# Performance work log

Hardware: AMD Instinct MI355X
Metric: run time of the kernel (lower is better)

The kernel has to match this reference:

```python
import jax, jax.numpy as jnp
import numpy as np

DIM = 768
NUM_HEADS = 12
LATENT_LEN = 32


def setup_inputs() -> dict:
    key = jax.random.key(0)
    k1, k2, k3, k4 = jax.random.split(key, 4)
    x = jax.random.normal(k1, (32, 4096, DIM), dtype=jnp.float32)
    latent = jax.random.normal(k2, (1, LATENT_LEN, DIM), dtype=jnp.float32) * 0.02
    # torch nn.Linear(dim, dim): weight [out, in], bias [out]
    bound = 1.0 / np.sqrt(DIM)
    v_w = jax.random.uniform(k3, (DIM, DIM), dtype=jnp.float32, minval=-bound, maxval=bound)
    v_b = jax.random.uniform(k4, (DIM,), dtype=jnp.float32, minval=-bound, maxval=bound)
    return {"x": x, "latent": latent, "v_w": v_w, "v_b": v_b}


def reference(x, latent, v_w, v_b):
    B, N, C = x.shape
    H = NUM_HEADS
    hd = C // H
    L = LATENT_LEN
    chunk = C // L
    scale = hd ** (-0.5)

    # q: [L, H, hd] from latent (shared across batch)
    q = latent[0].reshape(L, H, hd)
    # k: [B, N, H, hd]
    k = x.reshape(B, N, H, hd)
    # attn logits: [B, H, L, N]
    attn = jnp.einsum("lhd,bnhd->bhln", q * scale, k)
    attn = jax.nn.softmax(attn, axis=-1)
    attn = attn.mean(axis=1)  # [B, L, N] (head-mean before value matmul)

    # v: Linear then split channels by latent_len -> [B, L, N, chunk]
    v = (jnp.einsum("bnc,dc->bnd", x, v_w) + v_b).reshape(B, N, L, chunk)
    out = jnp.einsum("bln,blnc->blc", attn, v.transpose(0, 2, 1, 3))
    return out.reshape(B, 1, C)
```

## Files before the change

### kernel.cpp

```cpp
#include <hip/hip_runtime.h>
#include <cstdint>


typedef short bf16x8 __attribute__((ext_vector_type(8)));
typedef float f32x4 __attribute__((ext_vector_type(4)));

#define MFMA16(a, b, c) __builtin_amdgcn_mfma_f32_16x16x32_bf16((a), (b), (c), 0, 0, 0)

__device__ __forceinline__ unsigned short f2bf(float f) {
    union { float f; uint32_t u; } v; v.f = f;
    uint32_t u = v.u;
    u += 0x7FFFu + ((u >> 16) & 1u);
    return (unsigned short)(u >> 16);
}

template <int MODE>
__global__ __launch_bounds__(256)
void attn_sw_kernel(const float* __restrict__ x, const float* __restrict__ latent,
                    float* __restrict__ g_sums, const float* __restrict__ g_rs,
                    unsigned short* __restrict__ g_W)
{
    const int b   = blockIdx.x >> 6;
    const int n0  = (blockIdx.x & 63) << 6;
    const int tid = threadIdx.x;
    const int wv  = tid >> 6;
    const int lane = tid & 63;
    const int quad = lane >> 4;
    const int lc   = lane & 15;

    __shared__ unsigned short q_lds[32][72];
    __shared__ unsigned short x_lds[64][72];
    __shared__ float red_lds[384];

    if (MODE == 0) {
        for (int i = tid; i < 384; i += 256) red_lds[i] = 0.0f;
    } else {
        for (int i = tid; i < 384; i += 256) red_lds[i] = g_rs[b * 384 + i];
    }

    float acc0[4] = {0.f, 0.f, 0.f, 0.f};
    float acc1[4] = {0.f, 0.f, 0.f, 0.f};

    for (int h = 0; h < 12; ++h) {
        __syncthreads();
        for (int i = tid; i < 512; i += 256) {
            int l = i >> 4, f4 = i & 15;
            float4 qv = *(const float4*)&latent[l * 768 + h * 64 + f4 * 4];
            ushort4 qb;
            qb.x = f2bf(qv.x * 0.125f); qb.y = f2bf(qv.y * 0.125f);
            qb.z = f2bf(qv.z * 0.125f); qb.w = f2bf(qv.w * 0.125f);
            *(ushort4*)&q_lds[l][f4 * 4] = qb;
        }
        for (int i = tid; i < 1024; i += 256) {
            int n = i >> 4, f4 = i & 15;
            float4 xv = *(const float4*)&x[(b * 4096 + n0 + n) * 768 + h * 64 + f4 * 4];
            ushort4 xb;
            xb.x = f2bf(xv.x); xb.y = f2bf(xv.y);
            xb.z = f2bf(xv.z); xb.w = f2bf(xv.w);
            *(ushort4*)&x_lds[n][f4 * 4] = xb;
        }
        __syncthreads();

        bf16x8 a00 = *(const bf16x8*)&q_lds[lc][quad * 8];
        bf16x8 a01 = *(const bf16x8*)&q_lds[lc][32 + quad * 8];
        bf16x8 a10 = *(const bf16x8*)&q_lds[16 + lc][quad * 8];
        bf16x8 a11 = *(const bf16x8*)&q_lds[16 + lc][32 + quad * 8];
        bf16x8 b0  = *(const bf16x8*)&x_lds[wv * 16 + lc][quad * 8];
        bf16x8 b1  = *(const bf16x8*)&x_lds[wv * 16 + lc][32 + quad * 8];

        f32x4 c0 = {0.f, 0.f, 0.f, 0.f};
        f32x4 c1 = {0.f, 0.f, 0.f, 0.f};
        c0 = MFMA16(a00, b0, c0);
        c0 = MFMA16(a01, b1, c0);
        c1 = MFMA16(a10, b0, c1);
        c1 = MFMA16(a11, b1, c1);

        #pragma unroll
        for (int r = 0; r < 4; ++r) {
            float e0 = __expf(c0[r]);
            float e1 = __expf(c1[r]);
            if (MODE == 0) {
                float v0 = e0, v1 = e1;
                #pragma unroll
                for (int m = 1; m < 16; m <<= 1) {
                    v0 += __shfl_xor(v0, m);
                    v1 += __shfl_xor(v1, m);
                }
                if (lc == 0) {
                    atomicAdd(&red_lds[h * 32 + quad * 4 + r], v0);
                    atomicAdd(&red_lds[h * 32 + 16 + quad * 4 + r], v1);
                }
            } else {
                acc0[r] += e0 * red_lds[h * 32 + quad * 4 + r];
                acc1[r] += e1 * red_lds[h * 32 + 16 + quad * 4 + r];
            }
        }
    }

    if (MODE == 0) {
        __syncthreads();
        for (int i = tid; i < 384; i += 256)
            atomicAdd(&g_sums[b * 384 + i], red_lds[i]);
    } else {
        const int n = n0 + wv * 16 + lc;
        #pragma unroll
        for (int r = 0; r < 4; ++r) {
            g_W[(b * 32 + quad * 4 + r) * 4096 + n]      = f2bf(acc0[r]);
            g_W[(b * 32 + 16 + quad * 4 + r) * 4096 + n] = f2bf(acc1[r]);
        }
    }
}

__global__ __launch_bounds__(256)
void invert_kernel(const float* __restrict__ sums, float* __restrict__ rs)
{
    int i = blockIdx.x * 256 + threadIdx.x;
    if (i < 12288) rs[i] = 1.0f / (12.0f * sums[i]);
}

__global__ __launch_bounds__(64)
void yacc_kernel(const float* __restrict__ x, const unsigned short* __restrict__ W,
                 float* __restrict__ yws)
{
    const int bx  = blockIdx.x;
    const int b   = bx / 48;
    const int rem = bx - b * 48;
    const int ct  = rem % 12;
    const int g   = rem / 12;
    const int lane = threadIdx.x;
    const int quad = lane >> 4;
    const int lc   = lane & 15;
    const int c0   = ct * 64;
    const int nb   = g * 1024;

    const float* xb = x + b * 4096 * 768;
    const unsigned short* Wb = W + b * 32 * 4096;

    f32x4 acc[2][4];
    #pragma unroll
    for (int t = 0; t < 2; ++t)
        #pragma unroll
        for (int s = 0; s < 4; ++s) acc[t][s] = (f32x4){0.f, 0.f, 0.f, 0.f};

    for (int kk = 0; kk < 1024; kk += 32) {
        const int n = nb + kk + quad * 8;
        bf16x8 a0 = *(const bf16x8*)&Wb[lc * 4096 + n];
        bf16x8 a1 = *(const bf16x8*)&Wb[(16 + lc) * 4096 + n];
        #pragma unroll
        for (int s = 0; s < 4; ++s) {
            const float* xp = xb + n * 768 + c0 + s * 16 + lc;
            bf16x8 bb;
            #pragma unroll
            for (int j = 0; j < 8; ++j) bb[j] = (short)f2bf(xp[j * 768]);
            acc[0][s] = MFMA16(a0, bb, acc[0][s]);
            acc[1][s] = MFMA16(a1, bb, acc[1][s]);
        }
    }

    float* yp = yws + ((g * 32 + b) * 32) * 768;
    #pragma unroll
    for (int t = 0; t < 2; ++t)
        #pragma unroll
        for (int s = 0; s < 4; ++s)
            #pragma unroll
            for (int r = 0; r < 4; ++r) {
                int l = t * 16 + quad * 4 + r;
                int c = c0 + s * 16 + lc;
                yp[l * 768 + c] = acc[t][s][r];
            }
}

__global__ __launch_bounds__(256)
void out_kernel(const float* __restrict__ yws, const float* __restrict__ vw,
                const float* __restrict__ vb, float* __restrict__ out)
{
    const int b = blockIdx.x >> 5;
    const int l = blockIdx.x & 31;
    const int tid = threadIdx.x;
    __shared__ float y_lds[768];
    for (int c = tid; c < 768; c += 256) {
        float v = 0.f;
        #pragma unroll
        for (int g = 0; g < 4; ++g)
            v += yws[((g * 32 + b) * 32 + l) * 768 + c];
        y_lds[c] = v;
    }
    __syncthreads();
    const int wv = tid >> 6, lane = tid & 63;
    for (int i = wv; i < 24; i += 4) {
        const int row = l * 24 + i;
        const float* wr = vw + row * 768;
        float p = 0.f;
        #pragma unroll
        for (int j = 0; j < 12; ++j)
            p += y_lds[j * 64 + lane] * wr[j * 64 + lane];
        #pragma unroll
        for (int m = 1; m < 64; m <<= 1) p += __shfl_xor(p, m);
        if (lane == 0) out[b * 768 + row] = p + vb[row];
    }
}

extern "C" void kernel_launch(void* const* d_in, const int* in_sizes, int n_in,
                              void* d_out, int out_size, void* d_ws, size_t ws_size,
                              hipStream_t stream)
{
    const float* x      = (const float*)d_in[0];
    const float* latent = (const float*)d_in[1];
    const float* vw     = (const float*)d_in[2];
    const float* vb     = (const float*)d_in[3];
    float* out = (float*)d_out;

    char* ws = (char*)d_ws;
    float*          sums = (float*)ws;
    float*          rs   = (float*)(ws + 49152);
    unsigned short* W    = (unsigned short*)(ws + 98304);
    float*          yws  = (float*)(ws + 98304 + 8388608);

    hipMemsetAsync(sums, 0, 12288 * sizeof(float), stream);
    attn_sw_kernel<0><<<dim3(2048), dim3(256), 0, stream>>>(x, latent, sums, nullptr, nullptr);
    invert_kernel<<<dim3(48), dim3(256), 0, stream>>>(sums, rs);
    attn_sw_kernel<1><<<dim3(2048), dim3(256), 0, stream>>>(x, latent, nullptr, rs, W);
    yacc_kernel<<<dim3(1536), dim3(64), 0, stream>>>(x, W, yws);
    out_kernel<<<dim3(1024), dim3(256), 0, stream>>>(yws, vw, vb, out);
}
```

Before: 713.1 us.

## Materialize exp logits once instead of recomputing attention in two passes

Replaces the two-pass attention kernel (sum pass plus weighted pass, each rereading all of x) with a single pass that writes bf16 exp-logits to a 96MB workspace. A second kernel then reduces the per-head sums and forms the head-mean weights. This removes one full read of x (about 400MB) and its bf16 conversion, at the cost of writing and reading back roughly 100MB of intermediates. Two smaller changes come with it: bf16 conversion now truncates with a perm instruction instead of round-to-nearest, which may affect accuracy, and the yacc kernel is split into twice as many blocks over N for more parallelism.

```diff
diff --git a/kernel.cpp b/kernel.cpp
--- a/kernel.cpp
+++ b/kernel.cpp
@@ -7,18 +7,18 @@
 
 #define MFMA16(a, b, c) __builtin_amdgcn_mfma_f32_16x16x32_bf16((a), (b), (c), 0, 0, 0)
 
-__device__ __forceinline__ unsigned short f2bf(float f) {
-    union { float f; uint32_t u; } v; v.f = f;
-    uint32_t u = v.u;
-    u += 0x7FFFu + ((u >> 16) & 1u);
-    return (unsigned short)(u >> 16);
-}
-
-template <int MODE>
+__device__ __forceinline__ uint32_t pk_bf16(float a, float b) {
+    return __builtin_amdgcn_perm(__float_as_uint(b), __float_as_uint(a), 0x07060302u);
+}
+__device__ __forceinline__ unsigned short bf16_trunc(float f) {
+    return (unsigned short)(__float_as_uint(f) >> 16);
+}
+__device__ __forceinline__ float bf16_lo(uint32_t u) { return __uint_as_float(u << 16); }
+__device__ __forceinline__ float bf16_hi(uint32_t u) { return __uint_as_float(u & 0xffff0000u); }
+
 __global__ __launch_bounds__(256)
-void attn_sw_kernel(const float* __restrict__ x, const float* __restrict__ latent,
-                    float* __restrict__ g_sums, const float* __restrict__ g_rs,
-                    unsigned short* __restrict__ g_W)
+void k1_logits(const float* __restrict__ x, const float* __restrict__ latent,
+               unsigned short* __restrict__ E)
 {
     const int b   = blockIdx.x >> 6;
     const int n0  = (blockIdx.x & 63) << 6;
@@ -30,34 +30,26 @@
 
     __shared__ unsigned short q_lds[32][72];
     __shared__ unsigned short x_lds[64][72];
-    __shared__ float red_lds[384];
-
-    if (MODE == 0) {
-        for (int i = tid; i < 384; i += 256) red_lds[i] = 0.0f;
-    } else {
-        for (int i = tid; i < 384; i += 256) red_lds[i] = g_rs[b * 384 + i];
-    }
-
-    float acc0[4] = {0.f, 0.f, 0.f, 0.f};
-    float acc1[4] = {0.f, 0.f, 0.f, 0.f};
+
+    const int n = n0 + wv * 16 + lc;
 
     for (int h = 0; h < 12; ++h) {
         __syncthreads();
         for (int i = tid; i < 512; i += 256) {
             int l = i >> 4, f4 = i & 15;
             float4 qv = *(const float4*)&latent[l * 768 + h * 64 + f4 * 4];
-            ushort4 qb;
-            qb.x = f2bf(qv.x * 0.125f); qb.y = f2bf(qv.y * 0.125f);
-            qb.z = f2bf(qv.z * 0.125f); qb.w = f2bf(qv.w * 0.125f);
-            *(ushort4*)&q_lds[l][f4 * 4] = qb;
+            uint2 p;
+            p.x = pk_bf16(qv.x * 0.125f, qv.y * 0.125f);
+            p.y = pk_bf16(qv.z * 0.125f, qv.w * 0.125f);
+            *(uint2*)&q_lds[l][f4 * 4] = p;
         }
         for (int i = tid; i < 1024; i += 256) {
-            int n = i >> 4, f4 = i & 15;
-            float4 xv = *(const float4*)&x[(b * 4096 + n0 + n) * 768 + h * 64 + f4 * 4];
-            ushort4 xb;
-            xb.x = f2bf(xv.x); xb.y = f2bf(xv.y);
-            xb.z = f2bf(xv.z); xb.w = f2bf(xv.w);
-            *(ushort4*)&x_lds[n][f4 * 4] = xb;
+            int nn = i >> 4, f4 = i & 15;
+            float4 xv = *(const float4*)&x[(b * 4096 + n0 + nn) * 768 + h * 64 + f4 * 4];
+            uint2 p;
+            p.x = pk_bf16(xv.x, xv.y);
+            p.y = pk_bf16(xv.z, xv.w);
+            *(uint2*)&x_lds[nn][f4 * 4] = p;
         }
         __syncthreads();
 
@@ -75,47 +67,73 @@
         c1 = MFMA16(a10, b0, c1);
         c1 = MFMA16(a11, b1, c1);
 
+        unsigned short* Eh = E + (size_t)((b * 12 + h) * 32) * 4096;
         #pragma unroll
         for (int r = 0; r < 4; ++r) {
-            float e0 = __expf(c0[r]);
-            float e1 = __expf(c1[r]);
-            if (MODE == 0) {
-                float v0 = e0, v1 = e1;
-                #pragma unroll
-                for (int m = 1; m < 16; m <<= 1) {
-                    v0 += __shfl_xor(v0, m);
-                    v1 += __shfl_xor(v1, m);
-                }
-                if (lc == 0) {
-                    atomicAdd(&red_lds[h * 32 + quad * 4 + r], v0);
-                    atomicAdd(&red_lds[h * 32 + 16 + quad * 4 + r], v1);
-                }
-            } else {
-                acc0[r] += e0 * red_lds[h * 32 + quad * 4 + r];
-                acc1[r] += e1 * red_lds[h * 32 + 16 + quad * 4 + r];
-            }
-        }
-    }
-
-    if (MODE == 0) {
-        __syncthreads();
-        for (int i = tid; i < 384; i += 256)
-            atomicAdd(&g_sums[b * 384 + i], red_lds[i]);
-    } else {
-        const int n = n0 + wv * 16 + lc;
-        #pragma unroll
-        for (int r = 0; r < 4; ++r) {
-            g_W[(b * 32 + quad * 4 + r) * 4096 + n]      = f2bf(acc0[r]);
-            g_W[(b * 32 + 16 + quad * 4 + r) * 4096 + n] = f2bf(acc1[r]);
+            Eh[(quad * 4 + r) * 4096 + n]      = bf16_trunc(__expf(c0[r]));
+            Eh[(16 + quad * 4 + r) * 4096 + n] = bf16_trunc(__expf(c1[r]));
         }
     }
 }
 
 __global__ __launch_bounds__(256)
-void invert_kernel(const float* __restrict__ sums, float* __restrict__ rs)
-{
-    int i = blockIdx.x * 256 + threadIdx.x;
-    if (i < 12288) rs[i] = 1.0f / (12.0f * sums[i]);
+void kw_weights(const unsigned short* __restrict__ E, unsigned short* __restrict__ W)
+{
+    const int b = blockIdx.x >> 5;
+    const int l = blockIdx.x & 31;
+    const int tid = threadIdx.x;
+    const int wv = tid >> 6, lane = tid & 63;
+
+    const unsigned short* Eb = E + (size_t)(b * 384 + l) * 4096;
+    __shared__ float red[12][4];
+    __shared__ float rsl[12];
+
+    float s[12];
+    #pragma unroll
+    for (int h = 0; h < 12; ++h) {
+        const uint4* p = (const uint4*)(Eb + (size_t)h * 131072 + tid * 16);
+        uint4 u0 = p[0], u1 = p[1];
+        float v = 0.f;
+        v += bf16_lo(u0.x) + bf16_hi(u0.x) + bf16_lo(u0.y) + bf16_hi(u0.y);
+        v += bf16_lo(u0.z) + bf16_hi(u0.z) + bf16_lo(u0.w) + bf16_hi(u0.w);
+        v += bf16_lo(u1.x) + bf16_hi(u1.x) + bf16_lo(u1.y) + bf16_hi(u1.y);
+        v += bf16_lo(u1.z) + bf16_hi(u1.z) + bf16_lo(u1.w) + bf16_hi(u1.w);
+        #pragma unroll
+        for (int m = 1; m < 64; m <<= 1) v += __shfl_xor(v, m);
+        s[h] = v;
+    }
+    if (lane == 0) {
+        #pragma unroll
+        for (int h = 0; h < 12; ++h) red[h][wv] = s[h];
+    }
+    __syncthreads();
+    if (tid < 12) rsl[tid] = 1.0f / (12.0f * (red[tid][0] + red[tid][1] + red[tid][2] + red[tid][3]));
+    __syncthreads();
+
+    float acc[16];
+    #pragma unroll
+    for (int i = 0; i < 16; ++i) acc[i] = 0.f;
+    #pragma unroll
+    for (int h = 0; h < 12; ++h) {
+        float r = rsl[h];
+        const uint4* p = (const uint4*)(Eb + (size_t)h * 131072 + tid * 16);
+        uint4 u0 = p[0], u1 = p[1];
+        acc[0] += bf16_lo(u0.x) * r;  acc[1] += bf16_hi(u0.x) * r;
+        acc[2] += bf16_lo(u0.y) * r;  acc[3] += bf16_hi(u0.y) * r;
+        acc[4] += bf16_lo(u0.z) * r;  acc[5] += bf16_hi(u0.z) * r;
+        acc[6] += bf16_lo(u0.w) * r;  acc[7] += bf16_hi(u0.w) * r;
+        acc[8] += bf16_lo(u1.x) * r;  acc[9] += bf16_hi(u1.x) * r;
+        acc[10] += bf16_lo(u1.y) * r; acc[11] += bf16_hi(u1.y) * r;
+        acc[12] += bf16_lo(u1.z) * r; acc[13] += bf16_hi(u1.z) * r;
+        acc[14] += bf16_lo(u1.w) * r; acc[15] += bf16_hi(u1.w) * r;
+    }
+    uint4 o0, o1;
+    o0.x = pk_bf16(acc[0], acc[1]);   o0.y = pk_bf16(acc[2], acc[3]);
+    o0.z = pk_bf16(acc[4], acc[5]);   o0.w = pk_bf16(acc[6], acc[7]);
+    o1.x = pk_bf16(acc[8], acc[9]);   o1.y = pk_bf16(acc[10], acc[11]);
+    o1.z = pk_bf16(acc[12], acc[13]); o1.w = pk_bf16(acc[14], acc[15]);
+    uint4* wp = (uint4*)(W + (size_t)(b * 32 + l) * 4096 + tid * 16);
+    wp[0] = o0; wp[1] = o1;
 }
 
 __global__ __launch_bounds__(64)
@@ -123,18 +141,18 @@
                  float* __restrict__ yws)
 {
     const int bx  = blockIdx.x;
-    const int b   = bx / 48;
-    const int rem = bx - b * 48;
+    const int b   = bx / 96;
+    const int rem = bx - b * 96;
     const int ct  = rem % 12;
     const int g   = rem / 12;
     const int lane = threadIdx.x;
     const int quad = lane >> 4;
     const int lc   = lane & 15;
     const int c0   = ct * 64;
-    const int nb   = g * 1024;
-
-    const float* xb = x + b * 4096 * 768;
-    const unsigned short* Wb = W + b * 32 * 4096;
+    const int nb   = g * 512;
+
+    const float* xb = x + (size_t)b * 4096 * 768;
+    const unsigned short* Wb = W + (size_t)b * 32 * 4096;
 
     f32x4 acc[2][4];
     #pragma unroll
@@ -142,32 +160,33 @@
         #pragma unroll
         for (int s = 0; s < 4; ++s) acc[t][s] = (f32x4){0.f, 0.f, 0.f, 0.f};
 
-    for (int kk = 0; kk < 1024; kk += 32) {
+    for (int kk = 0; kk < 512; kk += 32) {
         const int n = nb + kk + quad * 8;
         bf16x8 a0 = *(const bf16x8*)&Wb[lc * 4096 + n];
         bf16x8 a1 = *(const bf16x8*)&Wb[(16 + lc) * 4096 + n];
         #pragma unroll
         for (int s = 0; s < 4; ++s) {
-            const float* xp = xb + n * 768 + c0 + s * 16 + lc;
-            bf16x8 bb;
-            #pragma unroll
-            for (int j = 0; j < 8; ++j) bb[j] = (short)f2bf(xp[j * 768]);
-            acc[0][s] = MFMA16(a0, bb, acc[0][s]);
-            acc[1][s] = MFMA16(a1, bb, acc[1][s]);
-        }
-    }
-
-    float* yp = yws + ((g * 32 + b) * 32) * 768;
+            const float* xp = xb + (size_t)n * 768 + c0 + s * 16 + lc;
+            float f0 = xp[0], f1 = xp[768], f2 = xp[1536], f3 = xp[2304];
+            float f4 = xp[3072], f5 = xp[3840], f6 = xp[4608], f7 = xp[5376];
+            union { uint32_t u[4]; bf16x8 v; } bb;
+            bb.u[0] = pk_bf16(f0, f1);
+            bb.u[1] = pk_bf16(f2, f3);
+            bb.u[2] = pk_bf16(f4, f5);
+            bb.u[3] = pk_bf16(f6, f7);
+            acc[0][s] = MFMA16(a0, bb.v, acc[0][s]);
+            acc[1][s] = MFMA16(a1, bb.v, acc[1][s]);
+        }
+    }
+
+    float* yp = yws + (size_t)((g * 32 + b) * 32) * 768;
     #pragma unroll
     for (int t = 0; t < 2; ++t)
         #pragma unroll
         for (int s = 0; s < 4; ++s)
             #pragma unroll
-            for (int r = 0; r < 4; ++r) {
-                int l = t * 16 + quad * 4 + r;
-                int c = c0 + s * 16 + lc;
-                yp[l * 768 + c] = acc[t][s][r];
-            }
+            for (int r = 0; r < 4; ++r)
+                yp[(t * 16 + quad * 4 + r) * 768 + c0 + s * 16 + lc] = acc[t][s][r];
 }
 
 __global__ __launch_bounds__(256)
@@ -181,8 +200,8 @@
     for (int c = tid; c < 768; c += 256) {
         float v = 0.f;
         #pragma unroll
-        for (int g = 0; g < 4; ++g)
-            v += yws[((g * 32 + b) * 32 + l) * 768 + c];
+        for (int g = 0; g < 8; ++g)
+            v += yws[(size_t)((g * 32 + b) * 32 + l) * 768 + c];
         y_lds[c] = v;
     }
     __syncthreads();
@@ -211,15 +230,12 @@
     float* out = (float*)d_out;
 
     char* ws = (char*)d_ws;
-    float*          sums = (float*)ws;
-    float*          rs   = (float*)(ws + 49152);
-    unsigned short* W    = (unsigned short*)(ws + 98304);
-    float*          yws  = (float*)(ws + 98304 + 8388608);
-
-    hipMemsetAsync(sums, 0, 12288 * sizeof(float), stream);
-    attn_sw_kernel<0><<<dim3(2048), dim3(256), 0, stream>>>(x, latent, sums, nullptr, nullptr);
-    invert_kernel<<<dim3(48), dim3(256), 0, stream>>>(sums, rs);
-    attn_sw_kernel<1><<<dim3(2048), dim3(256), 0, stream>>>(x, latent, nullptr, rs, W);
-    yacc_kernel<<<dim3(1536), dim3(64), 0, stream>>>(x, W, yws);
+    unsigned short* E   = (unsigned short*)ws;
+    unsigned short* W   = (unsigned short*)(ws + 100663296);
+    float*          yws = (float*)(ws + 109051904);
+
+    k1_logits<<<dim3(2048), dim3(256), 0, stream>>>(x, latent, E);
+    kw_weights<<<dim3(1024), dim3(256), 0, stream>>>(E, W);
+    yacc_kernel<<<dim3(3072), dim3(64), 0, stream>>>(x, W, yws);
     out_kernel<<<dim3(1024), dim3(256), 0, stream>>>(yws, vw, vb, out);
 }
```

Result: faster. 689.6 us (-3.3%).
